# Kernel tuning notes

Measured on AMD Instinct MI355X. Metric: run time of the kernel, lower is better.

Reference implementation:

```python
import jax, jax.numpy as jnp
from jax import lax
import numpy as np

B, S, D, H = 256, 2048, 16, 128
HH = H // 2  # head hidden = 64


def _p(key, shape, scale=0.05):
    return scale * jax.random.normal(key, shape, dtype=jnp.float32)


def setup_inputs() -> dict:
    key = jax.random.key(0)
    ks = jax.random.split(key, 12)
    return {
        "x": jax.random.normal(ks[0], (B, S, D), dtype=jnp.float32),
        # LSTM layer 0 (PyTorch gate order: i, f, g, o along the 4H axis)
        "W_ih0": _p(ks[1], (4 * H, D)),
        "W_hh0": _p(ks[2], (4 * H, H)),
        "b_ih0": jnp.zeros((4 * H,), jnp.float32),
        "b_hh0": jnp.zeros((4 * H,), jnp.float32),
        # LSTM layer 1
        "W_ih1": _p(ks[3], (4 * H, H)),
        "W_hh1": _p(ks[4], (4 * H, H)),
        "b_ih1": jnp.zeros((4 * H,), jnp.float32),
        "b_hh1": jnp.zeros((4 * H,), jnp.float32),
        # return head: Linear(H, H//2) -> LeakyReLU -> Linear(H//2, 1)
        "Wr1": _p(ks[5], (HH, H)), "br1": jnp.zeros((HH,), jnp.float32),
        "Wr2": _p(ks[6], (1, HH)), "br2": jnp.zeros((1,), jnp.float32),
        # vol head: Linear -> LeakyReLU -> Linear -> Softplus
        "Wv1": _p(ks[7], (HH, H)), "bv1": jnp.zeros((HH,), jnp.float32),
        "Wv2": _p(ks[8], (1, HH)), "bv2": jnp.zeros((1,), jnp.float32),
    }


def _lstm_layer(x, W_ih, W_hh, b_ih, b_hh):
    # x: (B, S, Din) -> hs: (B, S, H); PyTorch gate order i, f, g, o
    b, s, _ = x.shape
    h_dim = W_hh.shape[1]
    xg = jnp.einsum('bsd,gd->bsg', x, W_ih) + (b_ih + b_hh)  # (B, S, 4H)

    def step(carry, xg_t):
        h, c = carry
        g = xg_t + h @ W_hh.T
        i, f, gc, o = jnp.split(g, 4, axis=-1)
        i = jax.nn.sigmoid(i)
        f = jax.nn.sigmoid(f)
        gc = jnp.tanh(gc)
        o = jax.nn.sigmoid(o)
        c = f * c + i * gc
        h = o * jnp.tanh(c)
        return (h, c), h

    h0 = jnp.zeros((b, h_dim), x.dtype)
    (hN, cN), hs = lax.scan(step, (h0, jnp.zeros_like(h0)), jnp.swapaxes(xg, 0, 1))
    return jnp.swapaxes(hs, 0, 1), hN, cN


def reference(x, W_ih0, W_hh0, b_ih0, b_hh0, W_ih1, W_hh1, b_ih1, b_hh1,
              Wr1, br1, Wr2, br2, Wv1, bv1, Wv2, bv2):
    h1, hN0, cN0 = _lstm_layer(x, W_ih0, W_hh0, b_ih0, b_hh0)
    # inter-layer dropout is inactive at inference (eval mode)
    h2, hN1, cN1 = _lstm_layer(h1, W_ih1, W_hh1, b_ih1, b_hh1)
    # return head
    r = jax.nn.leaky_relu(jnp.einsum('bsh,kh->bsk', h2, Wr1) + br1)
    returns = jnp.einsum('bsk,ok->bso', r, Wr2) + br2
    # volatility head
    v = jax.nn.leaky_relu(jnp.einsum('bsh,kh->bsk', h2, Wv1) + bv1)
    volatility = jax.nn.softplus(jnp.einsum('bsk,ok->bso', v, Wv2) + bv2)
    hidden_h = jnp.stack([hN0, hN1], axis=0)  # (num_layers, B, H)
    hidden_c = jnp.stack([cN0, cN1], axis=0)
    return returns, volatility, hidden_h, hidden_c
```

## Files before the change

kernel.cpp:

```cpp
#include <hip/hip_runtime.h>
#include <hip/hip_bf16.h>

#define B_ 256
#define S_ 2048
#define D_ 16
#define H_ 128

typedef unsigned int u32;
typedef unsigned short u16;
typedef _Float16 h2t __attribute__((ext_vector_type(2)));

#define RET0 ((size_t)0)
#define VOL0 ((size_t)524288)
#define HH0  ((size_t)1048576)
#define HC0  ((size_t)1114112)

__device__ __forceinline__ float fdot2(u32 a, u32 b, float c) {
    return __builtin_amdgcn_fdot2(__builtin_bit_cast(h2t, a),
                                  __builtin_bit_cast(h2t, b), c, false);
}
__device__ __forceinline__ u32 packh2(float a, float b) {
    h2t h; h[0] = (_Float16)a; h[1] = (_Float16)b;
    return __builtin_bit_cast(u32, h);
}
__device__ __forceinline__ float sigm(float x) {
    return __builtin_amdgcn_rcpf(1.f + __builtin_amdgcn_exp2f(-1.44269504f * x));
}
__device__ __forceinline__ float tanh_(float x) {
    return 2.f * __builtin_amdgcn_rcpf(1.f + __builtin_amdgcn_exp2f(-2.88539008f * x)) - 1.f;
}
__device__ __forceinline__ float softplus_(float x) {
    if (x > 20.f) return x;
    const float e = __builtin_amdgcn_exp2f(1.44269504f * x);
    return 0.69314718f * __builtin_amdgcn_logf(1.f + e);
}
__device__ __forceinline__ float dxor1(float a) {
    return __builtin_bit_cast(float, __builtin_amdgcn_update_dpp(
        0, __builtin_bit_cast(int, a), 0xB1, 0xF, 0xF, true));
}
__device__ __forceinline__ float dxor2(float a) {
    return __builtin_bit_cast(float, __builtin_amdgcn_update_dpp(
        0, __builtin_bit_cast(int, a), 0x4E, 0xF, 0xF, true));
}
__device__ __forceinline__ float sxor4(float a) {
    return __builtin_bit_cast(float, __builtin_amdgcn_ds_swizzle(
        __builtin_bit_cast(int, a), 0x101F));
}
#define REDUCE8(a) { a += dxor1(a); a += dxor2(a); a += sxor4(a); }

__global__ __launch_bounds__(1024, 4) void k_l0(
    const float* __restrict__ x, const float* __restrict__ Wih,
    const float* __restrict__ Whh, const float* __restrict__ bih,
    const float* __restrict__ bhh, u32* __restrict__ h1out,
    float* __restrict__ out)
{
    __shared__ u32 xp2[2][4096];
    __shared__ u32 hb[2][64];
    __shared__ u32 och[4096];

    const int tid = threadIdx.x, b = blockIdx.x;
    const int m = tid >> 3, ksl = tid & 7;

    u32 wx[4], wh[32];
    float bias[4];
#pragma unroll
    for (int g = 0; g < 4; ++g) {
        const int row = g * H_ + m;
        const float2 f2 = *(const float2*)(Wih + row * D_ + ksl * 2);
        wx[g] = packh2(f2.x, f2.y);
        const float4* whr = (const float4*)(Whh + row * H_ + ksl * 16);
#pragma unroll
        for (int j = 0; j < 4; ++j) {
            const float4 f = whr[j];
            wh[g * 8 + 2 * j]     = packh2(f.x, f.y);
            wh[g * 8 + 2 * j + 1] = packh2(f.z, f.w);
        }
        bias[g] = bih[row] + bhh[row];
    }

    const float* xb = x + (size_t)b * S_ * D_;
    for (int i = tid; i < 2048; i += 1024) {
        const float4 v = *(const float4*)(xb + i * 4);
        xp2[0][2 * i] = packh2(v.x, v.y);
        xp2[0][2 * i + 1] = packh2(v.z, v.w);
    }
    if (tid < 128) ((u32*)hb)[tid] = 0u;
    float c = 0.f;
    __syncthreads();

    for (int t = 0; t < S_; ++t) {
        if ((t & 511) == 0 && t < S_ - 512) {
            const int nw = (t >> 9) + 1;
            u32* dst = xp2[nw & 1];
            const float* src = xb + (size_t)nw * 8192;
            for (int i = tid; i < 2048; i += 1024) {
                const float4 v = *(const float4*)(src + i * 4);
                dst[2 * i] = packh2(v.x, v.y);
                dst[2 * i + 1] = packh2(v.z, v.w);
            }
        }
        const u32 xv = xp2[(t >> 9) & 1][(t & 511) * 8 + ksl];
        const u32* hsel = &hb[(t + 1) & 1][ksl * 8];
        const uint4 h0 = *(const uint4*)(hsel);
        const uint4 h1v = *(const uint4*)(hsel + 4);

        float a0 = fdot2(xv, wx[0], 0.f), a1 = fdot2(xv, wx[1], 0.f);
        float a2 = fdot2(xv, wx[2], 0.f), a3 = fdot2(xv, wx[3], 0.f);
#define L0G(comp, j)                                                           \
        a0 = fdot2(comp, wh[j], a0);      a1 = fdot2(comp, wh[8 + (j)], a1);   \
        a2 = fdot2(comp, wh[16 + (j)], a2); a3 = fdot2(comp, wh[24 + (j)], a3);
        L0G(h0.x, 0) L0G(h0.y, 1) L0G(h0.z, 2) L0G(h0.w, 3)
        L0G(h1v.x, 4) L0G(h1v.y, 5) L0G(h1v.z, 6) L0G(h1v.w, 7)
#undef L0G
        REDUCE8(a0) REDUCE8(a1) REDUCE8(a2) REDUCE8(a3)
        const float ig = sigm(a0 + bias[0]);
        const float fg = sigm(a1 + bias[1]);
        const float gc = tanh_(a2 + bias[2]);
        const float og = sigm(a3 + bias[3]);
        c = fg * c + ig * gc;
        const float hv = og * tanh_(c);
        const u32 pp = packh2(hv, __shfl_xor(hv, 8));
        if ((tid & 15) == 0) {
            hb[t & 1][m >> 1] = pp;
            och[(t & 63) * 64 + (m >> 1)] = pp;
        }
        if (t == S_ - 1 && (tid & 7) == 0) {
            out[HH0 + (size_t)b * H_ + m] = hv;
            out[HC0 + (size_t)b * H_ + m] = c;
        }
        __syncthreads();
        if ((t & 63) == 63) {
            u32* dst = h1out + ((size_t)b * S_ + (t - 63)) * 64;
            *(uint4*)(dst + tid * 4) = *(const uint4*)(&och[tid * 4]);
            __syncthreads();
        }
    }
}

__global__ __launch_bounds__(1024, 4) void k_l1(
    u32* __restrict__ hws,
    const float* __restrict__ Wih, const float* __restrict__ Whh,
    const float* __restrict__ bih, const float* __restrict__ bhh,
    float* __restrict__ out)
{
    __shared__ u32 h1w[128 * 80];
    __shared__ u32 hp[2][80];
    __shared__ u32 och[4096];

    const int tid = threadIdx.x, b = blockIdx.x;
    const int m = tid >> 3, ksl = tid & 7;

    u32 w[64];
    float bias[4];
    const float* Wsel = (ksl < 4) ? Wih : Whh;
    const int colb = (ksl & 3) * 32;
#pragma unroll
    for (int g = 0; g < 4; ++g) {
        const int row = g * H_ + m;
        const float4* wr_ = (const float4*)(Wsel + row * H_ + colb);
#pragma unroll
        for (int j = 0; j < 8; ++j) {
            const float4 f = wr_[j];
            w[g * 16 + 2 * j]     = packh2(f.x, f.y);
            w[g * 16 + 2 * j + 1] = packh2(f.z, f.w);
        }
        bias[g] = bih[row] + bhh[row];
    }

    if (tid < 160) ((u32*)hp)[tid] = 0u;
    float c = 0.f;
    __syncthreads();

    u32* hbase = hws + (size_t)b * S_ * 64;
    for (int u = 0; u < S_; ++u) {
        if ((u & 127) == 0) {
            for (int i = tid; i < 2048; i += 1024) {
                const uint4 v = *(const uint4*)(hbase + (size_t)u * 64 + i * 4);
                const int st = i >> 4, p4 = i & 15;
                *(uint4*)(&h1w[st * 80 + (p4 >> 2) * 20 + (p4 & 3) * 4]) = v;
            }
            __syncthreads();
        }
        const u32* sel = (ksl < 4) ? &h1w[(u & 127) * 80 + ksl * 20]
                                   : &hp[(u + 1) & 1][(ksl - 4) * 20];
        float a0 = 0.f, a1 = 0.f, a2 = 0.f, a3 = 0.f;
#pragma unroll
        for (int p = 0; p < 4; ++p) {
            const uint4 v = *(const uint4*)(sel + p * 4);
            a0 = fdot2(v.x, w[4 * p], a0);      a0 = fdot2(v.y, w[4 * p + 1], a0);
            a0 = fdot2(v.z, w[4 * p + 2], a0);  a0 = fdot2(v.w, w[4 * p + 3], a0);
            a1 = fdot2(v.x, w[16 + 4 * p], a1); a1 = fdot2(v.y, w[17 + 4 * p], a1);
            a1 = fdot2(v.z, w[18 + 4 * p], a1); a1 = fdot2(v.w, w[19 + 4 * p], a1);
            a2 = fdot2(v.x, w[32 + 4 * p], a2); a2 = fdot2(v.y, w[33 + 4 * p], a2);
            a2 = fdot2(v.z, w[34 + 4 * p], a2); a2 = fdot2(v.w, w[35 + 4 * p], a2);
            a3 = fdot2(v.x, w[48 + 4 * p], a3); a3 = fdot2(v.y, w[49 + 4 * p], a3);
            a3 = fdot2(v.z, w[50 + 4 * p], a3); a3 = fdot2(v.w, w[51 + 4 * p], a3);
        }
        REDUCE8(a0) REDUCE8(a1) REDUCE8(a2) REDUCE8(a3)
        const float ig = sigm(a0 + bias[0]);
        const float fg = sigm(a1 + bias[1]);
        const float gc = tanh_(a2 + bias[2]);
        const float og = sigm(a3 + bias[3]);
        c = fg * c + ig * gc;
        const float hv = og * tanh_(c);
        const u32 pp = packh2(hv, __shfl_xor(hv, 8));
        if ((tid & 15) == 0) {
            const int m2 = m >> 1;
            hp[u & 1][(m2 >> 4) * 20 + (m2 & 15)] = pp;
            och[(u & 63) * 64 + m2] = pp;
        }
        if (u == S_ - 1 && (tid & 7) == 0) {
            out[HH0 + 32768 + (size_t)b * H_ + m] = hv;
            out[HC0 + 32768 + (size_t)b * H_ + m] = c;
        }
        __syncthreads();
        if ((u & 63) == 63) {
            u32* dst = hbase + (size_t)(u - 63) * 64;
            *(uint4*)(dst + tid * 4) = *(const uint4*)(&och[tid * 4]);
            __syncthreads();
        }
    }
}

__global__ __launch_bounds__(256) void k_heads(
    const u32* __restrict__ h2p,
    const float* __restrict__ Wr1, const float* __restrict__ br1,
    const float* __restrict__ Wr2, const float* __restrict__ br2,
    const float* __restrict__ Wv1, const float* __restrict__ bv1,
    const float* __restrict__ Wv2, const float* __restrict__ bv2,
    float* __restrict__ out)
{
    __shared__ u32 wr[64 * 64], wv[64 * 64];
    __shared__ float w2r[64], w2v[64], b1r[64], b1v[64];

    const int tid = threadIdx.x;
    for (int i = tid; i < 4096; i += 256) {
        wr[i] = packh2(Wr1[2 * i], Wr1[2 * i + 1]);
        wv[i] = packh2(Wv1[2 * i], Wv1[2 * i + 1]);
    }
    if (tid < 64) {
        w2r[tid] = Wr2[tid]; w2v[tid] = Wv2[tid];
        b1r[tid] = br1[tid]; b1v[tid] = bv1[tid];
    }
    __syncthreads();

    const size_t bs = (size_t)blockIdx.x * 256 + tid;
    u32 hq[64];
    const u32* src = h2p + bs * 64;
#pragma unroll
    for (int j4 = 0; j4 < 16; ++j4) {
        const uint4 v = *(const uint4*)(src + j4 * 4);
        hq[j4 * 4] = v.x; hq[j4 * 4 + 1] = v.y; hq[j4 * 4 + 2] = v.z; hq[j4 * 4 + 3] = v.w;
    }
    float ret = br2[0], vol = bv2[0];
    for (int k = 0; k < 64; ++k) {
        float r = b1r[k], v = b1v[k];
#pragma unroll
        for (int j = 0; j < 64; ++j) r = fdot2(hq[j], wr[k * 64 + j], r);
#pragma unroll
        for (int j = 0; j < 64; ++j) v = fdot2(hq[j], wv[k * 64 + j], v);
        r = r > 0.f ? r : 0.01f * r;
        v = v > 0.f ? v : 0.01f * v;
        ret += r * w2r[k];
        vol += v * w2v[k];
    }
    out[RET0 + bs] = ret;
    out[VOL0 + bs] = softplus_(vol);
}

extern "C" void kernel_launch(void* const* d_in, const int* in_sizes, int n_in,
                              void* d_out, int out_size, void* d_ws, size_t ws_size,
                              hipStream_t stream) {
    (void)in_sizes; (void)n_in; (void)out_size; (void)ws_size;
    const float* x    = (const float*)d_in[0];
    const float* Wih0 = (const float*)d_in[1];
    const float* Whh0 = (const float*)d_in[2];
    const float* bih0 = (const float*)d_in[3];
    const float* bhh0 = (const float*)d_in[4];
    const float* Wih1 = (const float*)d_in[5];
    const float* Whh1 = (const float*)d_in[6];
    const float* bih1 = (const float*)d_in[7];
    const float* bhh1 = (const float*)d_in[8];
    const float* Wr1  = (const float*)d_in[9];
    const float* br1  = (const float*)d_in[10];
    const float* Wr2  = (const float*)d_in[11];
    const float* br2  = (const float*)d_in[12];
    const float* Wv1  = (const float*)d_in[13];
    const float* bv1  = (const float*)d_in[14];
    const float* Wv2  = (const float*)d_in[15];
    const float* bv2  = (const float*)d_in[16];
    u32* hws = (u32*)d_ws;
    float* out = (float*)d_out;

    k_l0<<<B_, 1024, 0, stream>>>(x, Wih0, Whh0, bih0, bhh0, hws, out);
    k_l1<<<B_, 1024, 0, stream>>>(hws, Wih1, Whh1, bih1, bhh1, out);
    k_heads<<<2048, 256, 0, stream>>>(hws, Wr1, br1, Wr2, br2, Wv1, bv1, Wv2, bv2, out);
}
```

Baseline: 4.170 ms.

## Fuse both LSTM layers into one kernel with chunked producer-consumer flags

Merges the layer-0 and layer-1 kernels into a single 512-block launch. The first 256 blocks run layer 0 and publish a per-batch progress counter with release stores after each 64-step chunk of hidden states is written. The other 256 blocks run layer 1 and spin on that counter before loading each chunk, so the two recurrences can overlap instead of running back to back. The progress counters live in the output buffer and are zeroed by a small extra kernel. This depends on all blocks being co-resident and on dispatch order to avoid deadlock, and it adds spin-wait and fence overhead.

```diff
diff --git a/kernel.cpp b/kernel.cpp
--- a/kernel.cpp
+++ b/kernel.cpp
@@ -48,176 +48,191 @@
 }
 #define REDUCE8(a) { a += dxor1(a); a += dxor2(a); a += sxor4(a); }
 
-__global__ __launch_bounds__(1024, 4) void k_l0(
-    const float* __restrict__ x, const float* __restrict__ Wih,
-    const float* __restrict__ Whh, const float* __restrict__ bih,
-    const float* __restrict__ bhh, u32* __restrict__ h1out,
-    float* __restrict__ out)
+__global__ __launch_bounds__(256) void k_zero(u32* __restrict__ prog) {
+    prog[threadIdx.x] = 0u;
+}
+
+__global__ __launch_bounds__(1024, 4) void k_duo(
+    const float* __restrict__ x,
+    const float* __restrict__ Wih0, const float* __restrict__ Whh0,
+    const float* __restrict__ bih0, const float* __restrict__ bhh0,
+    const float* __restrict__ Wih1, const float* __restrict__ Whh1,
+    const float* __restrict__ bih1, const float* __restrict__ bhh1,
+    u32* __restrict__ hws, float* __restrict__ out, u32* __restrict__ prog)
 {
-    __shared__ u32 xp2[2][4096];
-    __shared__ u32 hb[2][64];
-    __shared__ u32 och[4096];
-
-    const int tid = threadIdx.x, b = blockIdx.x;
+    __shared__ u32 L[12416];
+
+    const int tid = threadIdx.x;
     const int m = tid >> 3, ksl = tid & 7;
 
-    u32 wx[4], wh[32];
-    float bias[4];
-#pragma unroll
-    for (int g = 0; g < 4; ++g) {
-        const int row = g * H_ + m;
-        const float2 f2 = *(const float2*)(Wih + row * D_ + ksl * 2);
-        wx[g] = packh2(f2.x, f2.y);
-        const float4* whr = (const float4*)(Whh + row * H_ + ksl * 16);
-#pragma unroll
-        for (int j = 0; j < 4; ++j) {
-            const float4 f = whr[j];
-            wh[g * 8 + 2 * j]     = packh2(f.x, f.y);
-            wh[g * 8 + 2 * j + 1] = packh2(f.z, f.w);
-        }
-        bias[g] = bih[row] + bhh[row];
-    }
-
-    const float* xb = x + (size_t)b * S_ * D_;
-    for (int i = tid; i < 2048; i += 1024) {
-        const float4 v = *(const float4*)(xb + i * 4);
-        xp2[0][2 * i] = packh2(v.x, v.y);
-        xp2[0][2 * i + 1] = packh2(v.z, v.w);
-    }
-    if (tid < 128) ((u32*)hb)[tid] = 0u;
-    float c = 0.f;
-    __syncthreads();
-
-    for (int t = 0; t < S_; ++t) {
-        if ((t & 511) == 0 && t < S_ - 512) {
-            const int nw = (t >> 9) + 1;
-            u32* dst = xp2[nw & 1];
-            const float* src = xb + (size_t)nw * 8192;
-            for (int i = tid; i < 2048; i += 1024) {
-                const float4 v = *(const float4*)(src + i * 4);
-                dst[2 * i] = packh2(v.x, v.y);
-                dst[2 * i + 1] = packh2(v.z, v.w);
-            }
-        }
-        const u32 xv = xp2[(t >> 9) & 1][(t & 511) * 8 + ksl];
-        const u32* hsel = &hb[(t + 1) & 1][ksl * 8];
-        const uint4 h0 = *(const uint4*)(hsel);
-        const uint4 h1v = *(const uint4*)(hsel + 4);
-
-        float a0 = fdot2(xv, wx[0], 0.f), a1 = fdot2(xv, wx[1], 0.f);
-        float a2 = fdot2(xv, wx[2], 0.f), a3 = fdot2(xv, wx[3], 0.f);
+    if (blockIdx.x < 256) {
+        const int b = blockIdx.x;
+        u32 (*xp2)[4096] = (u32(*)[4096]) & L[0];
+        u32 (*hb)[64] = (u32(*)[64]) & L[8192];
+        u32* och = &L[8320];
+
+        u32 wx[4], wh[32];
+        float bias[4];
+#pragma unroll
+        for (int g = 0; g < 4; ++g) {
+            const int row = g * H_ + m;
+            const float2 f2 = *(const float2*)(Wih0 + row * D_ + ksl * 2);
+            wx[g] = packh2(f2.x, f2.y);
+            const float4* whr = (const float4*)(Whh0 + row * H_ + ksl * 16);
+#pragma unroll
+            for (int j = 0; j < 4; ++j) {
+                const float4 f = whr[j];
+                wh[g * 8 + 2 * j]     = packh2(f.x, f.y);
+                wh[g * 8 + 2 * j + 1] = packh2(f.z, f.w);
+            }
+            bias[g] = bih0[row] + bhh0[row];
+        }
+
+        const float* xb = x + (size_t)b * S_ * D_;
+        for (int i = tid; i < 2048; i += 1024) {
+            const float4 v = *(const float4*)(xb + i * 4);
+            xp2[0][2 * i] = packh2(v.x, v.y);
+            xp2[0][2 * i + 1] = packh2(v.z, v.w);
+        }
+        if (tid < 128) ((u32*)hb)[tid] = 0u;
+        float c = 0.f;
+        __syncthreads();
+
+        for (int t = 0; t < S_; ++t) {
+            if ((t & 511) == 0 && t < S_ - 512) {
+                const int nw = (t >> 9) + 1;
+                u32* dst = xp2[nw & 1];
+                const float* src = xb + (size_t)nw * 8192;
+                for (int i = tid; i < 2048; i += 1024) {
+                    const float4 v = *(const float4*)(src + i * 4);
+                    dst[2 * i] = packh2(v.x, v.y);
+                    dst[2 * i + 1] = packh2(v.z, v.w);
+                }
+            }
+            const u32 xv = xp2[(t >> 9) & 1][(t & 511) * 8 + ksl];
+            const u32* hsel = &hb[(t + 1) & 1][ksl * 8];
+            const uint4 h0 = *(const uint4*)(hsel);
+            const uint4 h1v = *(const uint4*)(hsel + 4);
+
+            float a0 = fdot2(xv, wx[0], 0.f), a1 = fdot2(xv, wx[1], 0.f);
+            float a2 = fdot2(xv, wx[2], 0.f), a3 = fdot2(xv, wx[3], 0.f);
 #define L0G(comp, j)                                                           \
-        a0 = fdot2(comp, wh[j], a0);      a1 = fdot2(comp, wh[8 + (j)], a1);   \
-        a2 = fdot2(comp, wh[16 + (j)], a2); a3 = fdot2(comp, wh[24 + (j)], a3);
-        L0G(h0.x, 0) L0G(h0.y, 1) L0G(h0.z, 2) L0G(h0.w, 3)
-        L0G(h1v.x, 4) L0G(h1v.y, 5) L0G(h1v.z, 6) L0G(h1v.w, 7)
+            a0 = fdot2(comp, wh[j], a0);        a1 = fdot2(comp, wh[8 + (j)], a1); \
+            a2 = fdot2(comp, wh[16 + (j)], a2); a3 = fdot2(comp, wh[24 + (j)], a3);
+            L0G(h0.x, 0) L0G(h0.y, 1) L0G(h0.z, 2) L0G(h0.w, 3)
+            L0G(h1v.x, 4) L0G(h1v.y, 5) L0G(h1v.z, 6) L0G(h1v.w, 7)
 #undef L0G
-        REDUCE8(a0) REDUCE8(a1) REDUCE8(a2) REDUCE8(a3)
-        const float ig = sigm(a0 + bias[0]);
-        const float fg = sigm(a1 + bias[1]);
-        const float gc = tanh_(a2 + bias[2]);
-        const float og = sigm(a3 + bias[3]);
-        c = fg * c + ig * gc;
-        const float hv = og * tanh_(c);
-        const u32 pp = packh2(hv, __shfl_xor(hv, 8));
-        if ((tid & 15) == 0) {
-            hb[t & 1][m >> 1] = pp;
-            och[(t & 63) * 64 + (m >> 1)] = pp;
-        }
-        if (t == S_ - 1 && (tid & 7) == 0) {
-            out[HH0 + (size_t)b * H_ + m] = hv;
-            out[HC0 + (size_t)b * H_ + m] = c;
-        }
+            REDUCE8(a0) REDUCE8(a1) REDUCE8(a2) REDUCE8(a3)
+            const float ig = sigm(a0 + bias[0]);
+            const float fg = sigm(a1 + bias[1]);
+            const float gc = tanh_(a2 + bias[2]);
+            const float og = sigm(a3 + bias[3]);
+            c = fg * c + ig * gc;
+            const float hv = og * tanh_(c);
+            const u32 pp = packh2(hv, __shfl_xor(hv, 8));
+            if ((tid & 15) == 0) {
+                hb[t & 1][m >> 1] = pp;
+                och[(t & 63) * 64 + (m >> 1)] = pp;
+            }
+            if (t == S_ - 1 && (tid & 7) == 0) {
+                out[HH0 + (size_t)b * H_ + m] = hv;
+                out[HC0 + (size_t)b * H_ + m] = c;
+            }
+            __syncthreads();
+            if ((t & 63) == 63) {
+                u32* dst = hws + ((size_t)b * S_ + (t - 63)) * 64;
+                *(uint4*)(dst + tid * 4) = *(const uint4*)(&och[tid * 4]);
+                __syncthreads();
+                if (tid == 0) {
+                    __threadfence();
+                    __hip_atomic_store(&prog[b], (t >> 6) + 1,
+                                       __ATOMIC_RELEASE, __HIP_MEMORY_SCOPE_AGENT);
+                }
+            }
+        }
+    } else {
+        const int b = blockIdx.x - 256;
+        u32* h1w = &L[0];
+        u32 (*hp)[80] = (u32(*)[80]) & L[5120];
+        u32* och = &L[5280];
+
+        u32 w[64];
+        float bias[4];
+        const float* Wsel = (ksl < 4) ? Wih1 : Whh1;
+        const int colb = (ksl & 3) * 32;
+#pragma unroll
+        for (int g = 0; g < 4; ++g) {
+            const int row = g * H_ + m;
+            const float4* wr_ = (const float4*)(Wsel + row * H_ + colb);
+#pragma unroll
+            for (int j = 0; j < 8; ++j) {
+                const float4 f = wr_[j];
+                w[g * 16 + 2 * j]     = packh2(f.x, f.y);
+                w[g * 16 + 2 * j + 1] = packh2(f.z, f.w);
+            }
+            bias[g] = bih1[row] + bhh1[row];
+        }
+
+        if (tid < 160) ((u32*)hp)[tid] = 0u;
+        float c = 0.f;
         __syncthreads();
-        if ((t & 63) == 63) {
-            u32* dst = h1out + ((size_t)b * S_ + (t - 63)) * 64;
-            *(uint4*)(dst + tid * 4) = *(const uint4*)(&och[tid * 4]);
+
+        u32* hbase = hws + (size_t)b * S_ * 64;
+        for (int u = 0; u < S_; ++u) {
+            if ((u & 63) == 0) {
+                if (tid == 0) {
+                    const u32 need = (u >> 6) + 1;
+                    while (__hip_atomic_load(&prog[b], __ATOMIC_ACQUIRE,
+                                             __HIP_MEMORY_SCOPE_AGENT) < need)
+                        __builtin_amdgcn_s_sleep(32);
+                }
+                __syncthreads();
+                __threadfence();
+                {
+                    const uint4 v = *(const uint4*)(hbase + (size_t)u * 64 + tid * 4);
+                    const int st = tid >> 4, p4 = tid & 15;
+                    *(uint4*)(&h1w[st * 80 + (p4 >> 2) * 20 + (p4 & 3) * 4]) = v;
+                }
+                __syncthreads();
+            }
+            const u32* sel = (ksl < 4) ? &h1w[(u & 63) * 80 + ksl * 20]
+                                       : &hp[(u + 1) & 1][(ksl - 4) * 20];
+            float a0 = 0.f, a1 = 0.f, a2 = 0.f, a3 = 0.f;
+#pragma unroll
+            for (int p = 0; p < 4; ++p) {
+                const uint4 v = *(const uint4*)(sel + p * 4);
+                a0 = fdot2(v.x, w[4 * p], a0);      a0 = fdot2(v.y, w[4 * p + 1], a0);
+                a0 = fdot2(v.z, w[4 * p + 2], a0);  a0 = fdot2(v.w, w[4 * p + 3], a0);
+                a1 = fdot2(v.x, w[16 + 4 * p], a1); a1 = fdot2(v.y, w[17 + 4 * p], a1);
+                a1 = fdot2(v.z, w[18 + 4 * p], a1); a1 = fdot2(v.w, w[19 + 4 * p], a1);
+                a2 = fdot2(v.x, w[32 + 4 * p], a2); a2 = fdot2(v.y, w[33 + 4 * p], a2);
+                a2 = fdot2(v.z, w[34 + 4 * p], a2); a2 = fdot2(v.w, w[35 + 4 * p], a2);
+                a3 = fdot2(v.x, w[48 + 4 * p], a3); a3 = fdot2(v.y, w[49 + 4 * p], a3);
+                a3 = fdot2(v.z, w[50 + 4 * p], a3); a3 = fdot2(v.w, w[51 + 4 * p], a3);
+            }
+            REDUCE8(a0) REDUCE8(a1) REDUCE8(a2) REDUCE8(a3)
+            const float ig = sigm(a0 + bias[0]);
+            const float fg = sigm(a1 + bias[1]);
+            const float gc = tanh_(a2 + bias[2]);
+            const float og = sigm(a3 + bias[3]);
+            c = fg * c + ig * gc;
+            const float hv = og * tanh_(c);
+            const u32 pp = packh2(hv, __shfl_xor(hv, 8));
+            if ((tid & 15) == 0) {
+                const int m2 = m >> 1;
+                hp[u & 1][(m2 >> 4) * 20 + (m2 & 15)] = pp;
+                och[(u & 63) * 64 + m2] = pp;
+            }
+            if (u == S_ - 1 && (tid & 7) == 0) {
+                out[HH0 + 32768 + (size_t)b * H_ + m] = hv;
+                out[HC0 + 32768 + (size_t)b * H_ + m] = c;
+            }
             __syncthreads();
-        }
-    }
-}
-
-__global__ __launch_bounds__(1024, 4) void k_l1(
-    u32* __restrict__ hws,
-    const float* __restrict__ Wih, const float* __restrict__ Whh,
-    const float* __restrict__ bih, const float* __restrict__ bhh,
-    float* __restrict__ out)
-{
-    __shared__ u32 h1w[128 * 80];
-    __shared__ u32 hp[2][80];
-    __shared__ u32 och[4096];
-
-    const int tid = threadIdx.x, b = blockIdx.x;
-    const int m = tid >> 3, ksl = tid & 7;
-
-    u32 w[64];
-    float bias[4];
-    const float* Wsel = (ksl < 4) ? Wih : Whh;
-    const int colb = (ksl & 3) * 32;
-#pragma unroll
-    for (int g = 0; g < 4; ++g) {
-        const int row = g * H_ + m;
-        const float4* wr_ = (const float4*)(Wsel + row * H_ + colb);
-#pragma unroll
-        for (int j = 0; j < 8; ++j) {
-            const float4 f = wr_[j];
-            w[g * 16 + 2 * j]     = packh2(f.x, f.y);
-            w[g * 16 + 2 * j + 1] = packh2(f.z, f.w);
-        }
-        bias[g] = bih[row] + bhh[row];
-    }
-
-    if (tid < 160) ((u32*)hp)[tid] = 0u;
-    float c = 0.f;
-    __syncthreads();
-
-    u32* hbase = hws + (size_t)b * S_ * 64;
-    for (int u = 0; u < S_; ++u) {
-        if ((u & 127) == 0) {
-            for (int i = tid; i < 2048; i += 1024) {
-                const uint4 v = *(const uint4*)(hbase + (size_t)u * 64 + i * 4);
-                const int st = i >> 4, p4 = i & 15;
-                *(uint4*)(&h1w[st * 80 + (p4 >> 2) * 20 + (p4 & 3) * 4]) = v;
-            }
-            __syncthreads();
-        }
-        const u32* sel = (ksl < 4) ? &h1w[(u & 127) * 80 + ksl * 20]
-                                   : &hp[(u + 1) & 1][(ksl - 4) * 20];
-        float a0 = 0.f, a1 = 0.f, a2 = 0.f, a3 = 0.f;
-#pragma unroll
-        for (int p = 0; p < 4; ++p) {
-            const uint4 v = *(const uint4*)(sel + p * 4);
-            a0 = fdot2(v.x, w[4 * p], a0);      a0 = fdot2(v.y, w[4 * p + 1], a0);
-            a0 = fdot2(v.z, w[4 * p + 2], a0);  a0 = fdot2(v.w, w[4 * p + 3], a0);
-            a1 = fdot2(v.x, w[16 + 4 * p], a1); a1 = fdot2(v.y, w[17 + 4 * p], a1);
-            a1 = fdot2(v.z, w[18 + 4 * p], a1); a1 = fdot2(v.w, w[19 + 4 * p], a1);
-            a2 = fdot2(v.x, w[32 + 4 * p], a2); a2 = fdot2(v.y, w[33 + 4 * p], a2);
-            a2 = fdot2(v.z, w[34 + 4 * p], a2); a2 = fdot2(v.w, w[35 + 4 * p], a2);
-            a3 = fdot2(v.x, w[48 + 4 * p], a3); a3 = fdot2(v.y, w[49 + 4 * p], a3);
-            a3 = fdot2(v.z, w[50 + 4 * p], a3); a3 = fdot2(v.w, w[51 + 4 * p], a3);
-        }
-        REDUCE8(a0) REDUCE8(a1) REDUCE8(a2) REDUCE8(a3)
-        const float ig = sigm(a0 + bias[0]);
-        const float fg = sigm(a1 + bias[1]);
-        const float gc = tanh_(a2 + bias[2]);
-        const float og = sigm(a3 + bias[3]);
-        c = fg * c + ig * gc;
-        const float hv = og * tanh_(c);
-        const u32 pp = packh2(hv, __shfl_xor(hv, 8));
-        if ((tid & 15) == 0) {
-            const int m2 = m >> 1;
-            hp[u & 1][(m2 >> 4) * 20 + (m2 & 15)] = pp;
-            och[(u & 63) * 64 + m2] = pp;
-        }
-        if (u == S_ - 1 && (tid & 7) == 0) {
-            out[HH0 + 32768 + (size_t)b * H_ + m] = hv;
-            out[HC0 + 32768 + (size_t)b * H_ + m] = c;
-        }
-        __syncthreads();
-        if ((u & 63) == 63) {
-            u32* dst = hbase + (size_t)(u - 63) * 64;
-            *(uint4*)(dst + tid * 4) = *(const uint4*)(&och[tid * 4]);
-            __syncthreads();
+            if ((u & 63) == 63) {
+                u32* dst = hbase + (size_t)(u - 63) * 64;
+                *(uint4*)(dst + tid * 4) = *(const uint4*)(&och[tid * 4]);
+                __syncthreads();
+            }
         }
     }
 }
@@ -289,10 +304,13 @@
     const float* bv1  = (const float*)d_in[14];
     const float* Wv2  = (const float*)d_in[15];
     const float* bv2  = (const float*)d_in[16];
-    u32* hws = (u32*)d_ws;
+    u32* hws  = (u32*)d_ws;
     float* out = (float*)d_out;
-
-    k_l0<<<B_, 1024, 0, stream>>>(x, Wih0, Whh0, bih0, bhh0, hws, out);
-    k_l1<<<B_, 1024, 0, stream>>>(hws, Wih1, Whh1, bih1, bhh1, out);
-    k_heads<<<2048, 256, 0, stream>>>(hws, Wr1, br1, Wr2, br2, Wv1, bv1, Wv2, bv2, out);
-}
+    u32* prog = (u32*)d_out;
+
+    k_zero<<<1, 256, 0, stream>>>(prog);
+    k_duo<<<512, 1024, 0, stream>>>(x, Wih0, Whh0, bih0, bhh0,
+                                    Wih1, Whh1, bih1, bhh1, hws, out, prog);
+    k_heads<<<2048, 256, 0, stream>>>(hws, Wr1, br1, Wr2, br2,
+                                      Wv1, bv1, Wv2, bv2, out);
+}
```

New measurement: 5.473 ms. +31.2%, slower.

## Hoist layer-1 input projection out of recurrence into separate parallel kernel

Applied to the files above, without the earlier changes.

Layer 1's input-to-hidden projection moves into a new kernel, k_g1. It computes all timesteps' gate preactivations in fp16 up front and writes them to workspace. The recurrent kernel then only does the W_hh dot products, streaming the precomputed gates through double-buffered LDS, which halves per-step register weights and arithmetic on the serial critical path. The cross-lane reductions and the neighbour fetch swap ds_swizzle/shfl for DPP row_half_mirror/row_ror, and launch bounds change. This adds a large workspace round trip and fp16 rounding of the gate preactivations, and the new path runs only when the workspace is big enough.

```diff
diff --git a/kernel.cpp b/kernel.cpp
--- a/kernel.cpp
+++ b/kernel.cpp
@@ -15,6 +15,9 @@
 #define HH0  ((size_t)1048576)
 #define HC0  ((size_t)1114112)
 
+#define G1OFF ((size_t)33554432)
+#define WS_NEED 671088640ull
+
 __device__ __forceinline__ float fdot2(u32 a, u32 b, float c) {
     return __builtin_amdgcn_fdot2(__builtin_bit_cast(h2t, a),
                                   __builtin_bit_cast(h2t, b), c, false);
@@ -42,13 +45,17 @@
     return __builtin_bit_cast(float, __builtin_amdgcn_update_dpp(
         0, __builtin_bit_cast(int, a), 0x4E, 0xF, 0xF, true));
 }
-__device__ __forceinline__ float sxor4(float a) {
-    return __builtin_bit_cast(float, __builtin_amdgcn_ds_swizzle(
-        __builtin_bit_cast(int, a), 0x101F));
-}
-#define REDUCE8(a) { a += dxor1(a); a += dxor2(a); a += sxor4(a); }
-
-__global__ __launch_bounds__(1024, 4) void k_l0(
+__device__ __forceinline__ float dhalf(float a) {
+    return __builtin_bit_cast(float, __builtin_amdgcn_update_dpp(
+        0, __builtin_bit_cast(int, a), 0x141, 0xF, 0xF, true));
+}
+__device__ __forceinline__ float dror8(float a) {
+    return __builtin_bit_cast(float, __builtin_amdgcn_update_dpp(
+        0, __builtin_bit_cast(int, a), 0x128, 0xF, 0xF, true));
+}
+#define REDUCE8D(a) { a += dxor1(a); a += dxor2(a); a += dhalf(a); }
+
+__global__ __launch_bounds__(1024, 1) void k_l0(
     const float* __restrict__ x, const float* __restrict__ Wih,
     const float* __restrict__ Whh, const float* __restrict__ bih,
     const float* __restrict__ bhh, u32* __restrict__ h1out,
@@ -107,19 +114,19 @@
         float a0 = fdot2(xv, wx[0], 0.f), a1 = fdot2(xv, wx[1], 0.f);
         float a2 = fdot2(xv, wx[2], 0.f), a3 = fdot2(xv, wx[3], 0.f);
 #define L0G(comp, j)                                                           \
-        a0 = fdot2(comp, wh[j], a0);      a1 = fdot2(comp, wh[8 + (j)], a1);   \
+        a0 = fdot2(comp, wh[j], a0);        a1 = fdot2(comp, wh[8 + (j)], a1); \
         a2 = fdot2(comp, wh[16 + (j)], a2); a3 = fdot2(comp, wh[24 + (j)], a3);
         L0G(h0.x, 0) L0G(h0.y, 1) L0G(h0.z, 2) L0G(h0.w, 3)
         L0G(h1v.x, 4) L0G(h1v.y, 5) L0G(h1v.z, 6) L0G(h1v.w, 7)
 #undef L0G
-        REDUCE8(a0) REDUCE8(a1) REDUCE8(a2) REDUCE8(a3)
+        REDUCE8D(a0) REDUCE8D(a1) REDUCE8D(a2) REDUCE8D(a3)
         const float ig = sigm(a0 + bias[0]);
         const float fg = sigm(a1 + bias[1]);
         const float gc = tanh_(a2 + bias[2]);
         const float og = sigm(a3 + bias[3]);
         c = fg * c + ig * gc;
         const float hv = og * tanh_(c);
-        const u32 pp = packh2(hv, __shfl_xor(hv, 8));
+        const u32 pp = packh2(hv, dror8(hv));
         if ((tid & 15) == 0) {
             hb[t & 1][m >> 1] = pp;
             och[(t & 63) * 64 + (m >> 1)] = pp;
@@ -137,7 +144,133 @@
     }
 }
 
-__global__ __launch_bounds__(1024, 4) void k_l1(
+__global__ __launch_bounds__(1024, 1) void k_g1(
+    const u32* __restrict__ h1p, const float* __restrict__ Wih,
+    const float* __restrict__ bih, const float* __restrict__ bhh,
+    u32* __restrict__ g1)
+{
+    const int tid = threadIdx.x, b = blockIdx.x;
+    const int m = tid >> 3, ksl = tid & 7;
+
+    u32 w[32];
+    float bias[4];
+#pragma unroll
+    for (int g = 0; g < 4; ++g) {
+        const int row = g * H_ + m;
+        const float4* wr_ = (const float4*)(Wih + row * H_ + ksl * 16);
+#pragma unroll
+        for (int j = 0; j < 4; ++j) {
+            const float4 f = wr_[j];
+            w[g * 8 + 2 * j]     = packh2(f.x, f.y);
+            w[g * 8 + 2 * j + 1] = packh2(f.z, f.w);
+        }
+        bias[g] = bih[row] + bhh[row];
+    }
+
+    for (int t = 0; t < S_; ++t) {
+        const u32* hp_ = h1p + ((size_t)b * S_ + t) * 64 + ksl * 8;
+        const uint4 v0 = *(const uint4*)hp_;
+        const uint4 v1 = *(const uint4*)(hp_ + 4);
+        float a0 = 0.f, a1 = 0.f, a2 = 0.f, a3 = 0.f;
+#define G1G(comp, j)                                                           \
+        a0 = fdot2(comp, w[j], a0);        a1 = fdot2(comp, w[8 + (j)], a1);   \
+        a2 = fdot2(comp, w[16 + (j)], a2); a3 = fdot2(comp, w[24 + (j)], a3);
+        G1G(v0.x, 0) G1G(v0.y, 1) G1G(v0.z, 2) G1G(v0.w, 3)
+        G1G(v1.x, 4) G1G(v1.y, 5) G1G(v1.z, 6) G1G(v1.w, 7)
+#undef G1G
+        REDUCE8D(a0) REDUCE8D(a1) REDUCE8D(a2) REDUCE8D(a3)
+        if (ksl == 0) {
+            uint2 o;
+            o.x = packh2(a0 + bias[0], a1 + bias[1]);
+            o.y = packh2(a2 + bias[2], a3 + bias[3]);
+            *(uint2*)(g1 + (((size_t)b * S_ + t) * 128 + m) * 2) = o;
+        }
+    }
+}
+
+__global__ __launch_bounds__(1024, 1) void k_l1r(
+    u32* __restrict__ hws, const u32* __restrict__ g1,
+    const float* __restrict__ Whh, float* __restrict__ out)
+{
+    __shared__ u32 gbuf[2][8192];
+    __shared__ u32 hp[2][80];
+    __shared__ u32 och[4096];
+
+    const int tid = threadIdx.x, b = blockIdx.x;
+    const int m = tid >> 3, ksl = tid & 7;
+
+    u32 w[32];
+#pragma unroll
+    for (int g = 0; g < 4; ++g) {
+        const int row = g * H_ + m;
+        const float4* wr_ = (const float4*)(Whh + row * H_ + ksl * 16);
+#pragma unroll
+        for (int j = 0; j < 4; ++j) {
+            const float4 f = wr_[j];
+            w[g * 8 + 2 * j]     = packh2(f.x, f.y);
+            w[g * 8 + 2 * j + 1] = packh2(f.z, f.w);
+        }
+    }
+
+    if (tid < 160) ((u32*)hp)[tid] = 0u;
+    const u32* gsrc = g1 + (size_t)b * S_ * 256;
+    uint4 r0 = *(const uint4*)(gsrc + tid * 8);
+    uint4 r1 = *(const uint4*)(gsrc + tid * 8 + 4);
+    float c = 0.f;
+    __syncthreads();
+
+    u32* hbase = hws + (size_t)b * S_ * 64;
+    for (int u = 0; u < S_; ++u) {
+        if ((u & 31) == 0) {
+            const int cb = (u >> 5) & 1;
+            *(uint4*)(&gbuf[cb][tid * 8]) = r0;
+            *(uint4*)(&gbuf[cb][tid * 8 + 4]) = r1;
+            __syncthreads();
+            if (u + 32 < S_) {
+                r0 = *(const uint4*)(gsrc + (size_t)(u + 32) * 256 + tid * 8);
+                r1 = *(const uint4*)(gsrc + (size_t)(u + 32) * 256 + tid * 8 + 4);
+            }
+        }
+        const u32* sel = &hp[(u + 1) & 1][(ksl >> 1) * 20 + (ksl & 1) * 8];
+        const uint4 v0 = *(const uint4*)sel;
+        const uint4 v1 = *(const uint4*)(sel + 4);
+        float a0 = 0.f, a1 = 0.f, a2 = 0.f, a3 = 0.f;
+#define L1G(comp, j)                                                           \
+        a0 = fdot2(comp, w[j], a0);        a1 = fdot2(comp, w[8 + (j)], a1);   \
+        a2 = fdot2(comp, w[16 + (j)], a2); a3 = fdot2(comp, w[24 + (j)], a3);
+        L1G(v0.x, 0) L1G(v0.y, 1) L1G(v0.z, 2) L1G(v0.w, 3)
+        L1G(v1.x, 4) L1G(v1.y, 5) L1G(v1.z, 6) L1G(v1.w, 7)
+#undef L1G
+        REDUCE8D(a0) REDUCE8D(a1) REDUCE8D(a2) REDUCE8D(a3)
+        const uint2 gg = *(const uint2*)(&gbuf[(u >> 5) & 1][(u & 31) * 256 + m * 2]);
+        const h2t plo = __builtin_bit_cast(h2t, gg.x);
+        const h2t phi = __builtin_bit_cast(h2t, gg.y);
+        const float ig = sigm(a0 + (float)plo[0]);
+        const float fg = sigm(a1 + (float)plo[1]);
+        const float gc = tanh_(a2 + (float)phi[0]);
+        const float og = sigm(a3 + (float)phi[1]);
+        c = fg * c + ig * gc;
+        const float hv = og * tanh_(c);
+        const u32 pp = packh2(hv, dror8(hv));
+        if ((tid & 15) == 0) {
+            const int m2 = m >> 1;
+            hp[u & 1][(m2 >> 4) * 20 + (m2 & 15)] = pp;
+            och[(u & 63) * 64 + m2] = pp;
+        }
+        if (u == S_ - 1 && (tid & 7) == 0) {
+            out[HH0 + 32768 + (size_t)b * H_ + m] = hv;
+            out[HC0 + 32768 + (size_t)b * H_ + m] = c;
+        }
+        __syncthreads();
+        if ((u & 63) == 63) {
+            u32* dst = hbase + (size_t)(u - 63) * 64;
+            *(uint4*)(dst + tid * 4) = *(const uint4*)(&och[tid * 4]);
+            __syncthreads();
+        }
+    }
+}
+
+__global__ __launch_bounds__(1024, 1) void k_l1full(
     u32* __restrict__ hws,
     const float* __restrict__ Wih, const float* __restrict__ Whh,
     const float* __restrict__ bih, const float* __restrict__ bhh,
@@ -196,14 +329,14 @@
             a3 = fdot2(v.x, w[48 + 4 * p], a3); a3 = fdot2(v.y, w[49 + 4 * p], a3);
             a3 = fdot2(v.z, w[50 + 4 * p], a3); a3 = fdot2(v.w, w[51 + 4 * p], a3);
         }
-        REDUCE8(a0) REDUCE8(a1) REDUCE8(a2) REDUCE8(a3)
+        REDUCE8D(a0) REDUCE8D(a1) REDUCE8D(a2) REDUCE8D(a3)
         const float ig = sigm(a0 + bias[0]);
         const float fg = sigm(a1 + bias[1]);
         const float gc = tanh_(a2 + bias[2]);
         const float og = sigm(a3 + bias[3]);
         c = fg * c + ig * gc;
         const float hv = og * tanh_(c);
-        const u32 pp = packh2(hv, __shfl_xor(hv, 8));
+        const u32 pp = packh2(hv, dror8(hv));
         if ((tid & 15) == 0) {
             const int m2 = m >> 1;
             hp[u & 1][(m2 >> 4) * 20 + (m2 & 15)] = pp;
@@ -271,7 +404,7 @@
 extern "C" void kernel_launch(void* const* d_in, const int* in_sizes, int n_in,
                               void* d_out, int out_size, void* d_ws, size_t ws_size,
                               hipStream_t stream) {
-    (void)in_sizes; (void)n_in; (void)out_size; (void)ws_size;
+    (void)in_sizes; (void)n_in; (void)out_size;
     const float* x    = (const float*)d_in[0];
     const float* Wih0 = (const float*)d_in[1];
     const float* Whh0 = (const float*)d_in[2];
@@ -289,10 +422,17 @@
     const float* bv1  = (const float*)d_in[14];
     const float* Wv2  = (const float*)d_in[15];
     const float* bv2  = (const float*)d_in[16];
-    u32* hws = (u32*)d_ws;
+    u32* hws  = (u32*)d_ws;
     float* out = (float*)d_out;
 
     k_l0<<<B_, 1024, 0, stream>>>(x, Wih0, Whh0, bih0, bhh0, hws, out);
-    k_l1<<<B_, 1024, 0, stream>>>(hws, Wih1, Whh1, bih1, bhh1, out);
-    k_heads<<<2048, 256, 0, stream>>>(hws, Wr1, br1, Wr2, br2, Wv1, bv1, Wv2, bv2, out);
-}
+    if (ws_size >= WS_NEED) {
+        u32* g1 = hws + G1OFF;
+        k_g1<<<B_, 1024, 0, stream>>>(hws, Wih1, bih1, bhh1, g1);
+        k_l1r<<<B_, 1024, 0, stream>>>(hws, g1, Whh1, out);
+    } else {
+        k_l1full<<<B_, 1024, 0, stream>>>(hws, Wih1, Whh1, bih1, bhh1, out);
+    }
+    k_heads<<<2048, 256, 0, stream>>>(hws, Wr1, br1, Wr2, br2,
+                                      Wv1, bv1, Wv2, bv2, out);
+}
```

Result: faster. 4.013 ms (-3.8%).
